# Performance work log

Hardware: AMD Instinct MI355X
Metric: run time of the kernel (lower is better)

Reference implementation:

```python
import jax, jax.numpy as jnp
import numpy as np

B, S, DX, DM, H = 4, 2048, 1024, 1024, 16
DK = DM // H


def setup_inputs() -> dict:
    key = jax.random.key(0)
    ks = jax.random.split(key, 12)
    s = 0.02
    inp = {
        "q": jax.random.normal(ks[0], (B, S, DX), jnp.float32),
        "k": jax.random.normal(ks[1], (B, S, DX), jnp.float32),
        "v": jax.random.normal(ks[2], (B, S, DX), jnp.float32),
        "wq": jax.random.normal(ks[3], (DX, DM), jnp.float32) * s,
        "bq": jnp.zeros((DM,), jnp.float32),
        "wk": jax.random.normal(ks[4], (DX, DM), jnp.float32) * s,
        "bk": jnp.zeros((DM,), jnp.float32),
        "wv": jax.random.normal(ks[5], (DX, DM), jnp.float32) * s,
        "bv": jnp.zeros((DM,), jnp.float32),
        "wo": jax.random.normal(ks[6], (DM, DX), jnp.float32) * s,
        "bo": jnp.zeros((DX,), jnp.float32),
        # causal boolean mask [B, S_q, S_k]; True = attend
        "mask": jnp.broadcast_to(jnp.tril(jnp.ones((S, S), bool)), (B, S, S)),
    }
    return inp


def reference(q, k, v, wq, bq, wk, bk, wv, bv, wo, bo, mask):
    # Linear projections: [B,S,DX] @ [DX,DM] -> [B,S,DM]
    qh = (q @ wq + bq).reshape(B, S, H, DK).transpose(0, 2, 1, 3)  # [B,H,S,DK]
    kh = (k @ wk + bk).reshape(B, S, H, DK).transpose(0, 2, 1, 3)
    vh = (v @ wv + bv).reshape(B, S, H, DK).transpose(0, 2, 1, 3)

    scores = jnp.einsum("bhqd,bhkd->bhqk", qh, kh) / jnp.sqrt(jnp.float32(DK))
    neg = -jnp.finfo(scores.dtype).max
    scores = jnp.where(mask[:, None, :, :], scores, neg)  # mask.unsqueeze(1)
    p = jax.nn.softmax(scores, axis=-1)  # dropout inactive (eval / p=0)
    z = jnp.einsum("bhqk,bhkd->bhqd", p, vh)  # [B,H,S,DK]
    z = z.transpose(0, 2, 1, 3).reshape(B, S, DM)
    return z @ wo + bo
```

## Files before the change

kernel.cpp:

```cpp
#include <hip/hip_runtime.h>
#include <hip/hip_bf16.h>
#include <cstdint>

constexpr int Bb = 4, Sq = 2048, DXc = 1024, DMc = 1024, NH = 16, DKc = 64;
constexpr int GM = Bb * Sq;

typedef __attribute__((ext_vector_type(8))) short short8;
typedef __attribute__((ext_vector_type(4))) float f32x4;

__device__ inline unsigned short f2b(float f) {
  union { float f; uint32_t i; } c; c.f = f;
  uint32_t lsb = (c.i >> 16) & 1;
  c.i += 0x7fffu + lsb;
  return (unsigned short)(c.i >> 16);
}

__device__ inline uint32_t cvt_pk_bf16(float lo, float hi) {
  uint32_t r;
  asm("v_cvt_pk_bf16_f32 %0, %1, %2" : "=v"(r) : "v"(lo), "v"(hi));
  return r;
}

__device__ inline void load16_lds(const unsigned short* g, unsigned short* l) {
  __builtin_amdgcn_global_load_lds(
      (const __attribute__((address_space(1))) void*)g,
      (__attribute__((address_space(3))) void*)l, 16, 0, 0);
}

__device__ inline void xcd_map(int d, int& m0, int& n0) {
  const int c = d & 7, k = d >> 3;
  n0 = (k & 7) * 128;
  m0 = (c * 8 + (k >> 3)) * 128;
}

__global__ __launch_bounds__(256) void wt4_k(
    const float* __restrict__ wq, const float* __restrict__ wk,
    const float* __restrict__ wv, const float* __restrict__ wo,
    unsigned short* __restrict__ wqt, unsigned short* __restrict__ wkt,
    unsigned short* __restrict__ wvt, unsigned short* __restrict__ wot) {
  const int z = blockIdx.z;
  const float* W = z == 0 ? wq : z == 1 ? wk : z == 2 ? wv : wo;
  unsigned short* WT = z == 0 ? wqt : z == 1 ? wkt : z == 2 ? wvt : wot;
  __shared__ float t[64][65];
  const int tid = threadIdx.x;
  const int k0 = blockIdx.y * 64, n0 = blockIdx.x * 64;
#pragma unroll
  for (int p = 0; p < 4; ++p) {
    const int c = tid + p * 256;
    const int r = c >> 4, c4 = (c & 15) << 2;
    float4 v = *(const float4*)&W[(size_t)(k0 + r) * 1024 + n0 + c4];
    t[r][c4 + 0] = v.x; t[r][c4 + 1] = v.y; t[r][c4 + 2] = v.z; t[r][c4 + 3] = v.w;
  }
  __syncthreads();
#pragma unroll
  for (int p = 0; p < 4; ++p) {
    const int c = tid + p * 256;
    const int n = c >> 4, k4 = (c & 15) << 2;
    ushort4 o;
    o.x = f2b(t[k4 + 0][n]); o.y = f2b(t[k4 + 1][n]);
    o.z = f2b(t[k4 + 2][n]); o.w = f2b(t[k4 + 3][n]);
    *(ushort4*)&WT[(size_t)(n0 + n) * 1024 + k0 + k4] = o;
  }
}

__global__ __launch_bounds__(256) void qkv_k(
    const float* __restrict__ q, const float* __restrict__ k,
    const float* __restrict__ v,
    const unsigned short* __restrict__ wqt, const unsigned short* __restrict__ wkt,
    const unsigned short* __restrict__ wvt,
    const float* __restrict__ bq, const float* __restrict__ bk,
    const float* __restrict__ bv,
    unsigned short* __restrict__ qh, unsigned short* __restrict__ kh,
    unsigned short* __restrict__ vh) {
  constexpr int K = 1024;
  __shared__ __align__(16) unsigned short As[128 * 32];
  __shared__ __align__(16) unsigned short Bs[128 * 32];
  const int z = blockIdx.y;
  const float* A = z == 0 ? q : z == 1 ? k : v;
  const unsigned short* BT = z == 0 ? wqt : z == 1 ? wkt : wvt;
  const float* bias = z == 0 ? bq : z == 1 ? bk : bv;
  unsigned short* outB = z == 0 ? qh : z == 1 ? kh : vh;

  const int tid = threadIdx.x;
  const int lane = tid & 63;
  const int quad = lane >> 4, l16 = lane & 15;
  const int w = tid >> 6;
  const int wrow = (w >> 1) * 64, wcol = (w & 1) * 64;
  int m0, n0;
  xcd_map(blockIdx.x, m0, n0);

  const int s0 = tid, s1 = tid + 256;
  const int ar0 = s0 >> 2, ac0 = (s0 & 3) * 8;
  const int ar1 = s1 >> 2, ac1 = (s1 & 3) * 8;

  f32x4 acc[4][4];
#pragma unroll
  for (int i = 0; i < 4; ++i)
#pragma unroll
    for (int j = 0; j < 4; ++j) acc[i][j] = (f32x4){0.f, 0.f, 0.f, 0.f};

  for (int k0 = 0; k0 < K; k0 += 32) {
    __syncthreads();
#pragma unroll
    for (int p = 0; p < 2; ++p) {
      const int c = tid + p * 256;
      const int row = c >> 2, ks = (c & 3) << 3;
      load16_lds(&BT[(size_t)(n0 + row) * K + k0 + ks], &Bs[c * 8]);
    }
    const float4 a0 = *(const float4*)&A[(size_t)(m0 + ar0) * K + k0 + ac0];
    const float4 a1 = *(const float4*)&A[(size_t)(m0 + ar0) * K + k0 + ac0 + 4];
    const float4 a2 = *(const float4*)&A[(size_t)(m0 + ar1) * K + k0 + ac1];
    const float4 a3 = *(const float4*)&A[(size_t)(m0 + ar1) * K + k0 + ac1 + 4];
    {
      uint4 p0, p1;
      p0.x = cvt_pk_bf16(a0.x, a0.y); p0.y = cvt_pk_bf16(a0.z, a0.w);
      p0.z = cvt_pk_bf16(a1.x, a1.y); p0.w = cvt_pk_bf16(a1.z, a1.w);
      p1.x = cvt_pk_bf16(a2.x, a2.y); p1.y = cvt_pk_bf16(a2.z, a2.w);
      p1.z = cvt_pk_bf16(a3.x, a3.y); p1.w = cvt_pk_bf16(a3.z, a3.w);
      *(uint4*)&As[s0 * 8] = p0;
      *(uint4*)&As[s1 * 8] = p1;
    }
    __syncthreads();

    short8 af[4], bf[4];
#pragma unroll
    for (int i = 0; i < 4; ++i)
      af[i] = *(const short8*)&As[(wrow + i * 16 + l16) * 32 + quad * 8];
#pragma unroll
    for (int j = 0; j < 4; ++j)
      bf[j] = *(const short8*)&Bs[(wcol + j * 16 + l16) * 32 + quad * 8];
#pragma unroll
    for (int i = 0; i < 4; ++i)
#pragma unroll
      for (int j = 0; j < 4; ++j)
        acc[i][j] = __builtin_amdgcn_mfma_f32_16x16x32_bf16(af[i], bf[j], acc[i][j], 0, 0, 0);
  }

  float bvv[4];
#pragma unroll
  for (int j = 0; j < 4; ++j) bvv[j] = bias[n0 + wcol + j * 16 + l16];
#pragma unroll
  for (int i = 0; i < 4; ++i)
#pragma unroll
    for (int j = 0; j < 4; ++j)
#pragma unroll
      for (int r = 0; r < 4; ++r) {
        const int m = m0 + wrow + i * 16 + quad * 4 + r;
        const int n = n0 + wcol + j * 16 + l16;
        const float val = acc[i][j][r] + bvv[j];
        const int b = m >> 11, s = m & 2047, h = n >> 6, d = n & 63;
        if (z < 2) {
          outB[(((size_t)(b * NH + h) * Sq + s) << 6) + d] = f2b(val);
        } else {
          outB[(((size_t)(b * NH + h) * DKc + d) << 11) + s] = f2b(val);
        }
      }
}

__global__ __launch_bounds__(256) void mgemm_o(
    const unsigned short* __restrict__ A, const unsigned short* __restrict__ BT,
    const float* __restrict__ bias, float* __restrict__ outF) {
  constexpr int K = 1024;
  __shared__ __align__(16) unsigned short As[128 * 32];
  __shared__ __align__(16) unsigned short Bs[128 * 32];
  const int tid = threadIdx.x;
  const int lane = tid & 63;
  const int quad = lane >> 4, l16 = lane & 15;
  const int w = tid >> 6;
  const int wrow = (w >> 1) * 64, wcol = (w & 1) * 64;
  int m0, n0;
  xcd_map(blockIdx.x, m0, n0);

  f32x4 acc[4][4];
#pragma unroll
  for (int i = 0; i < 4; ++i)
#pragma unroll
    for (int j = 0; j < 4; ++j) acc[i][j] = (f32x4){0.f, 0.f, 0.f, 0.f};

  for (int k0 = 0; k0 < K; k0 += 32) {
    __syncthreads();
#pragma unroll
    for (int p = 0; p < 2; ++p) {
      const int c = tid + p * 256;
      const int row = c >> 2, ks = (c & 3) << 3;
      load16_lds(&A[(size_t)(m0 + row) * K + k0 + ks], &As[c * 8]);
      load16_lds(&BT[(size_t)(n0 + row) * K + k0 + ks], &Bs[c * 8]);
    }
    __syncthreads();

    short8 af[4], bf[4];
#pragma unroll
    for (int i = 0; i < 4; ++i)
      af[i] = *(const short8*)&As[(wrow + i * 16 + l16) * 32 + quad * 8];
#pragma unroll
    for (int j = 0; j < 4; ++j)
      bf[j] = *(const short8*)&Bs[(wcol + j * 16 + l16) * 32 + quad * 8];
#pragma unroll
    for (int i = 0; i < 4; ++i)
#pragma unroll
      for (int j = 0; j < 4; ++j)
        acc[i][j] = __builtin_amdgcn_mfma_f32_16x16x32_bf16(af[i], bf[j], acc[i][j], 0, 0, 0);
  }

  float bv[4];
#pragma unroll
  for (int j = 0; j < 4; ++j) bv[j] = bias[n0 + wcol + j * 16 + l16];
#pragma unroll
  for (int i = 0; i < 4; ++i)
#pragma unroll
    for (int j = 0; j < 4; ++j)
#pragma unroll
      for (int r = 0; r < 4; ++r) {
        const int m = m0 + wrow + i * 16 + quad * 4 + r;
        const int n = n0 + wcol + j * 16 + l16;
        outF[(size_t)m * 1024 + n] = acc[i][j][r] + bv[j];
      }
}

__global__ __launch_bounds__(512) void flash_k(
    const unsigned short* __restrict__ Qh, const unsigned short* __restrict__ Kh,
    const unsigned short* __restrict__ Vt, unsigned short* __restrict__ Zb) {
  constexpr int LDP = 72;
  __shared__ __align__(16) unsigned short Klds[64 * 64];
  __shared__ __align__(16) unsigned short Vlds[64 * 64];
  __shared__ __align__(16) unsigned short Plds[8 * 16 * LDP];
  const int tid = threadIdx.x;
  const int w = tid >> 6, lane = tid & 63;
  const int quad = lane >> 4, l16 = lane & 15;
  const int bh = blockIdx.x & 63;
  const int qi = blockIdx.x >> 6;
  const int qa = qi * 128;
  const int qbv = (15 - qi) * 128;
  const size_t base = (size_t)bh * Sq * DKc;
  unsigned short* Pw = &Plds[w * 16 * LDP];

  const int qb[2] = {qa + w * 16, qbv + (7 - w) * 16};
  const int tiles_s[2] = {2 * qi + 1 + (w >= 4 ? 1 : 0),
                          31 - 2 * qi + (w < 4 ? 1 : 0)};
  const int ntile = 32 - 2 * qi;

  short8 qf0[2], qf1[2];
#pragma unroll
  for (int s = 0; s < 2; ++s) {
    const unsigned short* qp = Qh + base + (size_t)(qb[s] + l16) * DKc + quad * 8;
    qf0[s] = *(const short8*)qp;
    qf1[s] = *(const short8*)(qp + 32);
  }

  f32x4 oacc[2][4];
#pragma unroll
  for (int s = 0; s < 2; ++s)
#pragma unroll
    for (int n = 0; n < 4; ++n) oacc[s][n] = (f32x4){0.f, 0.f, 0.f, 0.f};
  float lsum[2] = {0.f, 0.f};

  const int row0 = tid >> 3, sp0 = tid & 7, gs0 = sp0 ^ (row0 & 7);
  const int pos0 = quad ^ (l16 & 7);
  const int pos1 = pos0 ^ 4;

  for (int it = 0; it < ntile; ++it) {
    const int kt0 = it * 64;
    __syncthreads();
    load16_lds(Kh + base + (size_t)(kt0 + row0) * DKc + gs0 * 8, &Klds[tid * 8]);
    load16_lds(Vt + base + (size_t)row0 * Sq + kt0 + gs0 * 8, &Vlds[tid * 8]);
    __syncthreads();

    short8 kf0[4], kf1[4];
#pragma unroll
    for (int t = 0; t < 4; ++t) {
      const int krow = (t * 16 + l16) * 64;
      kf0[t] = *(const short8*)&Klds[krow + pos0 * 8];
      kf1[t] = *(const short8*)&Klds[krow + pos1 * 8];
    }

#pragma unroll
    for (int s = 0; s < 2; ++s) {
      if (it >= tiles_s[s]) continue;
      f32x4 st[4];
#pragma unroll
      for (int t = 0; t < 4; ++t) {
        f32x4 z4 = (f32x4){0.f, 0.f, 0.f, 0.f};
        z4 = __builtin_amdgcn_mfma_f32_16x16x32_bf16(kf0[t], qf0[s], z4, 0, 0, 0);
        st[t] = __builtin_amdgcn_mfma_f32_16x16x32_bf16(kf1[t], qf1[s], z4, 0, 0, 0);
      }
      const int qrow = qb[s] + l16;
      float p[4][4];
      if (it == tiles_s[s] - 1) {
#pragma unroll
        for (int t = 0; t < 4; ++t)
#pragma unroll
          for (int r = 0; r < 4; ++r) {
            const int key = kt0 + t * 16 + quad * 4 + r;
            const float e = __expf(fminf(st[t][r] * 0.125f, 30.f));
            p[t][r] = (key <= qrow) ? e : 0.f;
          }
      } else {
#pragma unroll
        for (int t = 0; t < 4; ++t)
#pragma unroll
          for (int r = 0; r < 4; ++r)
            p[t][r] = __expf(fminf(st[t][r] * 0.125f, 30.f));
      }
#pragma unroll
      for (int t = 0; t < 4; ++t)
#pragma unroll
        for (int r = 0; r < 4; ++r) lsum[s] += p[t][r];
#pragma unroll
      for (int t = 0; t < 4; ++t) {
        ushort4 pk;
        pk.x = f2b(p[t][0]); pk.y = f2b(p[t][1]);
        pk.z = f2b(p[t][2]); pk.w = f2b(p[t][3]);
        *(ushort4*)&Pw[l16 * LDP + t * 16 + quad * 4] = pk;
      }
      short8 pf0 = *(const short8*)&Pw[l16 * LDP + quad * 8];
      short8 pf1 = *(const short8*)&Pw[l16 * LDP + 32 + quad * 8];
#pragma unroll
      for (int n = 0; n < 4; ++n) {
        const int vrow = (n * 16 + l16) * 64;
        short8 vf0 = *(const short8*)&Vlds[vrow + pos0 * 8];
        short8 vf1 = *(const short8*)&Vlds[vrow + pos1 * 8];
        oacc[s][n] = __builtin_amdgcn_mfma_f32_16x16x32_bf16(pf0, vf0, oacc[s][n], 0, 0, 0);
        oacc[s][n] = __builtin_amdgcn_mfma_f32_16x16x32_bf16(pf1, vf1, oacc[s][n], 0, 0, 0);
      }
    }
  }

  const int b = bh >> 4, h = bh & 15;
#pragma unroll
  for (int s = 0; s < 2; ++s) {
    float ls = lsum[s];
    ls += __shfl_xor(ls, 16, 64);
    ls += __shfl_xor(ls, 32, 64);
    const float inv = 1.f / ls;
    float invr[4];
#pragma unroll
    for (int r = 0; r < 4; ++r) invr[r] = __shfl(inv, quad * 4 + r, 64);
#pragma unroll
    for (int r = 0; r < 4; ++r) {
      const int row = qb[s] + quad * 4 + r;
      unsigned short* zp = Zb + ((size_t)b * Sq + row) * DMc + h * 64;
#pragma unroll
      for (int n = 0; n < 4; ++n) zp[n * 16 + l16] = f2b(oacc[s][n][r] * invr[r]);
    }
  }
}

extern "C" void kernel_launch(void* const* d_in, const int* in_sizes, int n_in,
                              void* d_out, int out_size, void* d_ws, size_t ws_size,
                              hipStream_t stream) {
  const float* q  = (const float*)d_in[0];
  const float* k  = (const float*)d_in[1];
  const float* v  = (const float*)d_in[2];
  const float* wq = (const float*)d_in[3];
  const float* bq = (const float*)d_in[4];
  const float* wk = (const float*)d_in[5];
  const float* bk = (const float*)d_in[6];
  const float* wv = (const float*)d_in[7];
  const float* bv = (const float*)d_in[8];
  const float* wo = (const float*)d_in[9];
  const float* bo = (const float*)d_in[10];

  constexpr size_t NEL = (size_t)GM * DMc;
  unsigned short* qh  = (unsigned short*)d_ws;
  unsigned short* kh  = qh + NEL;
  unsigned short* vh  = kh + NEL;
  unsigned short* xbf = vh + NEL;
  unsigned short* wqt = xbf + NEL;
  unsigned short* wkt = wqt + (size_t)DXc * DMc;
  unsigned short* wvt = wkt + (size_t)DXc * DMc;
  unsigned short* wot = wvt + (size_t)DXc * DMc;

  wt4_k<<<dim3(16, 16, 4), 256, 0, stream>>>(wq, wk, wv, wo, wqt, wkt, wvt, wot);
  qkv_k<<<dim3(512, 3), 256, 0, stream>>>(q, k, v, wqt, wkt, wvt,
                                          bq, bk, bv, qh, kh, vh);
  flash_k<<<dim3(512), 512, 0, stream>>>(qh, kh, vh, xbf);
  mgemm_o<<<dim3(512), 256, 0, stream>>>(xbf, wot, bo, (float*)d_out);
}
```

Before: 410.1 us.

## Double-buffer LDS tiles in QKV and output projection GEMMs

Both projection GEMM kernels now keep two LDS buffers for the A and B tiles. The next k-slice is prefetched, via global_load_lds or register loads with bf16 conversion, while MFMAs run on the current slice. This cuts one barrier per iteration and hides global-memory latency behind compute. In exchange, LDS use per block doubles to 32 KB, which may reduce occupancy, and the QKV kernel holds extra registers for the prefetched float4 values.

Result: faster. 391.7 us (-4.5%).

```diff
diff --git a/kernel.cpp b/kernel.cpp
--- a/kernel.cpp
+++ b/kernel.cpp
@@ -73,8 +73,8 @@
     unsigned short* __restrict__ qh, unsigned short* __restrict__ kh,
     unsigned short* __restrict__ vh) {
   constexpr int K = 1024;
-  __shared__ __align__(16) unsigned short As[128 * 32];
-  __shared__ __align__(16) unsigned short Bs[128 * 32];
+  __shared__ __align__(16) unsigned short As[2][128 * 32];
+  __shared__ __align__(16) unsigned short Bs[2][128 * 32];
   const int z = blockIdx.y;
   const float* A = z == 0 ? q : z == 1 ? k : v;
   const unsigned short* BT = z == 0 ? wqt : z == 1 ? wkt : wvt;
@@ -92,6 +92,8 @@
   const int s0 = tid, s1 = tid + 256;
   const int ar0 = s0 >> 2, ac0 = (s0 & 3) * 8;
   const int ar1 = s1 >> 2, ac1 = (s1 & 3) * 8;
+  const int br0 = s0 >> 2, bk0 = (s0 & 3) << 3;
+  const int br1 = s1 >> 2, bk1 = (s1 & 3) << 3;
 
   f32x4 acc[4][4];
 #pragma unroll
@@ -99,41 +101,59 @@
 #pragma unroll
     for (int j = 0; j < 4; ++j) acc[i][j] = (f32x4){0.f, 0.f, 0.f, 0.f};
 
-  for (int k0 = 0; k0 < K; k0 += 32) {
-    __syncthreads();
-#pragma unroll
-    for (int p = 0; p < 2; ++p) {
-      const int c = tid + p * 256;
-      const int row = c >> 2, ks = (c & 3) << 3;
-      load16_lds(&BT[(size_t)(n0 + row) * K + k0 + ks], &Bs[c * 8]);
-    }
-    const float4 a0 = *(const float4*)&A[(size_t)(m0 + ar0) * K + k0 + ac0];
-    const float4 a1 = *(const float4*)&A[(size_t)(m0 + ar0) * K + k0 + ac0 + 4];
-    const float4 a2 = *(const float4*)&A[(size_t)(m0 + ar1) * K + k0 + ac1];
-    const float4 a3 = *(const float4*)&A[(size_t)(m0 + ar1) * K + k0 + ac1 + 4];
-    {
+  load16_lds(&BT[(size_t)(n0 + br0) * K + bk0], &Bs[0][s0 * 8]);
+  load16_lds(&BT[(size_t)(n0 + br1) * K + bk1], &Bs[0][s1 * 8]);
+  {
+    const float4 a0 = *(const float4*)&A[(size_t)(m0 + ar0) * K + ac0];
+    const float4 a1 = *(const float4*)&A[(size_t)(m0 + ar0) * K + ac0 + 4];
+    const float4 a2 = *(const float4*)&A[(size_t)(m0 + ar1) * K + ac1];
+    const float4 a3 = *(const float4*)&A[(size_t)(m0 + ar1) * K + ac1 + 4];
+    uint4 p0, p1;
+    p0.x = cvt_pk_bf16(a0.x, a0.y); p0.y = cvt_pk_bf16(a0.z, a0.w);
+    p0.z = cvt_pk_bf16(a1.x, a1.y); p0.w = cvt_pk_bf16(a1.z, a1.w);
+    p1.x = cvt_pk_bf16(a2.x, a2.y); p1.y = cvt_pk_bf16(a2.z, a2.w);
+    p1.z = cvt_pk_bf16(a3.x, a3.y); p1.w = cvt_pk_bf16(a3.z, a3.w);
+    *(uint4*)&As[0][s0 * 8] = p0;
+    *(uint4*)&As[0][s1 * 8] = p1;
+  }
+  __syncthreads();
+
+  for (int t = 0; t < 32; ++t) {
+    const int cur = t & 1, nxt = cur ^ 1;
+    float4 a0, a1, a2, a3;
+    if (t < 31) {
+      const int kn = (t + 1) * 32;
+      load16_lds(&BT[(size_t)(n0 + br0) * K + kn + bk0], &Bs[nxt][s0 * 8]);
+      load16_lds(&BT[(size_t)(n0 + br1) * K + kn + bk1], &Bs[nxt][s1 * 8]);
+      a0 = *(const float4*)&A[(size_t)(m0 + ar0) * K + kn + ac0];
+      a1 = *(const float4*)&A[(size_t)(m0 + ar0) * K + kn + ac0 + 4];
+      a2 = *(const float4*)&A[(size_t)(m0 + ar1) * K + kn + ac1];
+      a3 = *(const float4*)&A[(size_t)(m0 + ar1) * K + kn + ac1 + 4];
+    }
+
+    short8 af[4], bf[4];
+#pragma unroll
+    for (int i = 0; i < 4; ++i)
+      af[i] = *(const short8*)&As[cur][(wrow + i * 16 + l16) * 32 + quad * 8];
+#pragma unroll
+    for (int j = 0; j < 4; ++j)
+      bf[j] = *(const short8*)&Bs[cur][(wcol + j * 16 + l16) * 32 + quad * 8];
+#pragma unroll
+    for (int i = 0; i < 4; ++i)
+#pragma unroll
+      for (int j = 0; j < 4; ++j)
+        acc[i][j] = __builtin_amdgcn_mfma_f32_16x16x32_bf16(af[i], bf[j], acc[i][j], 0, 0, 0);
+
+    if (t < 31) {
       uint4 p0, p1;
       p0.x = cvt_pk_bf16(a0.x, a0.y); p0.y = cvt_pk_bf16(a0.z, a0.w);
       p0.z = cvt_pk_bf16(a1.x, a1.y); p0.w = cvt_pk_bf16(a1.z, a1.w);
       p1.x = cvt_pk_bf16(a2.x, a2.y); p1.y = cvt_pk_bf16(a2.z, a2.w);
       p1.z = cvt_pk_bf16(a3.x, a3.y); p1.w = cvt_pk_bf16(a3.z, a3.w);
-      *(uint4*)&As[s0 * 8] = p0;
-      *(uint4*)&As[s1 * 8] = p1;
+      *(uint4*)&As[nxt][s0 * 8] = p0;
+      *(uint4*)&As[nxt][s1 * 8] = p1;
     }
     __syncthreads();
-
-    short8 af[4], bf[4];
-#pragma unroll
-    for (int i = 0; i < 4; ++i)
-      af[i] = *(const short8*)&As[(wrow + i * 16 + l16) * 32 + quad * 8];
-#pragma unroll
-    for (int j = 0; j < 4; ++j)
-      bf[j] = *(const short8*)&Bs[(wcol + j * 16 + l16) * 32 + quad * 8];
-#pragma unroll
-    for (int i = 0; i < 4; ++i)
-#pragma unroll
-      for (int j = 0; j < 4; ++j)
-        acc[i][j] = __builtin_amdgcn_mfma_f32_16x16x32_bf16(af[i], bf[j], acc[i][j], 0, 0, 0);
   }
 
   float bvv[4];
@@ -161,8 +181,8 @@
     const unsigned short* __restrict__ A, const unsigned short* __restrict__ BT,
     const float* __restrict__ bias, float* __restrict__ outF) {
   constexpr int K = 1024;
-  __shared__ __align__(16) unsigned short As[128 * 32];
-  __shared__ __align__(16) unsigned short Bs[128 * 32];
+  __shared__ __align__(16) unsigned short As[2][128 * 32];
+  __shared__ __align__(16) unsigned short Bs[2][128 * 32];
   const int tid = threadIdx.x;
   const int lane = tid & 63;
   const int quad = lane >> 4, l16 = lane & 15;
@@ -171,35 +191,46 @@
   int m0, n0;
   xcd_map(blockIdx.x, m0, n0);
 
+  const int s0 = tid, s1 = tid + 256;
+  const int r0 = s0 >> 2, c0 = (s0 & 3) << 3;
+  const int r1 = s1 >> 2, c1 = (s1 & 3) << 3;
+
   f32x4 acc[4][4];
 #pragma unroll
   for (int i = 0; i < 4; ++i)
 #pragma unroll
     for (int j = 0; j < 4; ++j) acc[i][j] = (f32x4){0.f, 0.f, 0.f, 0.f};
 
-  for (int k0 = 0; k0 < K; k0 += 32) {
-    __syncthreads();
-#pragma unroll
-    for (int p = 0; p < 2; ++p) {
-      const int c = tid + p * 256;
-      const int row = c >> 2, ks = (c & 3) << 3;
-      load16_lds(&A[(size_t)(m0 + row) * K + k0 + ks], &As[c * 8]);
-      load16_lds(&BT[(size_t)(n0 + row) * K + k0 + ks], &Bs[c * 8]);
-    }
-    __syncthreads();
+  load16_lds(&A[(size_t)(m0 + r0) * K + c0], &As[0][s0 * 8]);
+  load16_lds(&A[(size_t)(m0 + r1) * K + c1], &As[0][s1 * 8]);
+  load16_lds(&BT[(size_t)(n0 + r0) * K + c0], &Bs[0][s0 * 8]);
+  load16_lds(&BT[(size_t)(n0 + r1) * K + c1], &Bs[0][s1 * 8]);
+  __syncthreads();
+
+  for (int t = 0; t < 32; ++t) {
+    const int cur = t & 1, nxt = cur ^ 1;
+    if (t < 31) {
+      const int kn = (t + 1) * 32;
+      load16_lds(&A[(size_t)(m0 + r0) * K + kn + c0], &As[nxt][s0 * 8]);
+      load16_lds(&A[(size_t)(m0 + r1) * K + kn + c1], &As[nxt][s1 * 8]);
+      load16_lds(&BT[(size_t)(n0 + r0) * K + kn + c0], &Bs[nxt][s0 * 8]);
+      load16_lds(&BT[(size_t)(n0 + r1) * K + kn + c1], &Bs[nxt][s1 * 8]);
+    }
 
     short8 af[4], bf[4];
 #pragma unroll
     for (int i = 0; i < 4; ++i)
-      af[i] = *(const short8*)&As[(wrow + i * 16 + l16) * 32 + quad * 8];
+      af[i] = *(const short8*)&As[cur][(wrow + i * 16 + l16) * 32 + quad * 8];
 #pragma unroll
     for (int j = 0; j < 4; ++j)
-      bf[j] = *(const short8*)&Bs[(wcol + j * 16 + l16) * 32 + quad * 8];
+      bf[j] = *(const short8*)&Bs[cur][(wcol + j * 16 + l16) * 32 + quad * 8];
 #pragma unroll
     for (int i = 0; i < 4; ++i)
 #pragma unroll
       for (int j = 0; j < 4; ++j)
         acc[i][j] = __builtin_amdgcn_mfma_f32_16x16x32_bf16(af[i], bf[j], acc[i][j], 0, 0, 0);
+
+    __syncthreads();
   }
 
   float bv[4];
```
